# Performance work log

Measured on AMD Instinct MI355X. Metric: run time of the kernel, lower is better.

## Reference

```python
import jax, jax.numpy as jnp
import numpy as np

H = 1024   # hidden size
NH = 16    # num attention heads
HD = H // NH  # head dim = 64


def setup_inputs() -> dict:
    key = jax.random.key(0)
    ks = jax.random.split(key, 8)
    B, S = 2, 2048
    scale = 0.02
    return {
        "hidden_states": jax.random.normal(ks[0], (B, S, H), dtype=jnp.float32),
        "attention_mask": jnp.zeros((B, 1, 1, S), dtype=jnp.float32),
        "Wq": jax.random.normal(ks[1], (H, H), dtype=jnp.float32) * scale,
        "bq": jnp.zeros((H,), dtype=jnp.float32),
        "Wk": jax.random.normal(ks[2], (H, H), dtype=jnp.float32) * scale,
        "bk": jnp.zeros((H,), dtype=jnp.float32),
        "Wv": jax.random.normal(ks[3], (H, H), dtype=jnp.float32) * scale,
        "bv": jnp.zeros((H,), dtype=jnp.float32),
    }


def reference(hidden_states, attention_mask, Wq, bq, Wk, bk, Wv, bv):
    B, S, _ = hidden_states.shape

    def split_heads(x):  # [B,S,H] -> [B,NH,S,HD]
        return x.reshape(B, S, NH, HD).transpose(0, 2, 1, 3)

    q = split_heads(hidden_states @ Wq.T + bq)
    k = split_heads(hidden_states @ Wk.T + bk)
    v = split_heads(hidden_states @ Wv.T + bv)

    # raw attention scores [B,NH,S,S]
    scores = jnp.einsum("bhqd,bhkd->bhqk", q, k) / jnp.sqrt(jnp.float32(HD))
    scores = scores + attention_mask  # additive mask, broadcast [B,1,1,S]
    probs = jax.nn.softmax(scores, axis=-1)
    # dropout(p=0.1) is identity in eval mode

    ctx = jnp.einsum("bhqk,bhkd->bhqd", probs, v)  # [B,NH,S,HD]
    return ctx.transpose(0, 2, 1, 3).reshape(B, S, H)
```

## Files before the change

### kernel.cpp

```cpp
#include <hip/hip_runtime.h>
#include <hip/hip_bf16.h>
#include <math.h>

#define HSZ 1024
#define NHD 16
#define SEQ 2048
#define BSZ 2
#define MTOT (BSZ*SEQ)

typedef __attribute__((ext_vector_type(4)))  float  f32x4;
typedef __attribute__((ext_vector_type(8)))  __bf16 bf16x8;

#define LOG2E 1.4426950408889634f

#if __has_builtin(__builtin_amdgcn_exp2f)
#define EXP2(x) __builtin_amdgcn_exp2f(x)
#else
#define EXP2(x) exp2f(x)
#endif

__device__ __forceinline__ unsigned short f2bf(float x) {
    union { float f; unsigned u; } v; v.f = x;
    unsigned r = v.u + 0x7FFFu + ((v.u >> 16) & 1u);
    return (unsigned short)(r >> 16);
}
__device__ __forceinline__ unsigned cvtpk(float lo, float hi) {
    unsigned r;
    asm("v_cvt_pk_bf16_f32 %0, %1, %2" : "=v"(r) : "v"(lo), "v"(hi));
    return r;
}

__global__ __launch_bounds__(256) void cvt_all(
    const float* __restrict__ h,  unsigned short* __restrict__ hd,
    const float* __restrict__ w0, unsigned short* __restrict__ w0d,
    const float* __restrict__ w1, unsigned short* __restrict__ w1d,
    const float* __restrict__ w2, unsigned short* __restrict__ w2d)
{
    const float* s; unsigned short* d; int i;
    const int bid = blockIdx.x;
    if (bid < 2048)      { s = h;  d = hd;  i = bid; }
    else if (bid < 2560) { s = w0; d = w0d; i = bid - 2048; }
    else if (bid < 3072) { s = w1; d = w1d; i = bid - 2560; }
    else                 { s = w2; d = w2d; i = bid - 3072; }
    const int o = (i * 256 + threadIdx.x) * 8;
    float4 a = *(const float4*)(s + o);
    float4 b = *(const float4*)(s + o + 4);
    uint4 v;
    v.x = f2bf(a.x) | ((unsigned)f2bf(a.y) << 16);
    v.y = f2bf(a.z) | ((unsigned)f2bf(a.w) << 16);
    v.z = f2bf(b.x) | ((unsigned)f2bf(b.y) << 16);
    v.w = f2bf(b.z) | ((unsigned)f2bf(b.w) << 16);
    *(uint4*)(d + o) = v;
}

__global__ __launch_bounds__(256) void qkv_gemm(
    const unsigned short* __restrict__ hb,
    const unsigned short* __restrict__ wq,
    const unsigned short* __restrict__ wk,
    const unsigned short* __restrict__ wv,
    const float* __restrict__ bq, const float* __restrict__ bk,
    const float* __restrict__ bv,
    unsigned short* __restrict__ qo, char* __restrict__ ko,
    char* __restrict__ vo)
{
    __shared__ __align__(16) unsigned short As[128 * 32];
    __shared__ __align__(16) unsigned short Bs[128 * 32];

    const int t = threadIdx.x;
    const int w = t >> 6, l = t & 63, g = l >> 4, c = l & 15;
    const int bn = blockIdx.x, bm = blockIdx.y;
    const int which = bn >> 3;
    const int n0 = (bn & 7) << 7;
    const int m0 = bm << 7;
    const unsigned short* W = (which == 0) ? wq : (which == 1) ? wk : wv;
    const float* bb = (which == 0) ? bq : (which == 1) ? bk : bv;
    const float scale = (which == 0) ? 0.125f * LOG2E : 1.0f;
    const int wr = w >> 1, wc = w & 1;

    f32x4 acc[4][4];
    #pragma unroll
    for (int mi = 0; mi < 4; ++mi)
        #pragma unroll
        for (int ni = 0; ni < 4; ++ni) acc[mi][ni] = {0.f, 0.f, 0.f, 0.f};

    for (int k0 = 0; k0 < HSZ; k0 += 32) {
        #pragma unroll
        for (int i2 = 0; i2 < 2; ++i2) {
            const int chunk = 2 * w + i2;
            const int row = (chunk << 4) + (l >> 2);
            const int sg = (l & 3) ^ ((row >> 1) & 3);
            const char* ga = (const char*)hb +
                (((size_t)(m0 + row) << 10) + k0) * 2 + sg * 16;
            const char* gb = (const char*)W +
                (((size_t)(n0 + row) << 10) + k0) * 2 + sg * 16;
            __builtin_amdgcn_global_load_lds(
                (const __attribute__((address_space(1))) unsigned*)ga,
                (__attribute__((address_space(3))) unsigned*)((char*)As + chunk * 1024),
                16, 0, 0);
            __builtin_amdgcn_global_load_lds(
                (const __attribute__((address_space(1))) unsigned*)gb,
                (__attribute__((address_space(3))) unsigned*)((char*)Bs + chunk * 1024),
                16, 0, 0);
        }
        __syncthreads();

        bf16x8 af[4], bfr[4];
        #pragma unroll
        for (int mi = 0; mi < 4; ++mi) {
            const int row = wr * 64 + mi * 16 + c;
            const int gg = g ^ ((row >> 1) & 3);
            af[mi] = *(const bf16x8*)((const char*)As + row * 64 + gg * 16);
        }
        #pragma unroll
        for (int ni = 0; ni < 4; ++ni) {
            const int row = wc * 64 + ni * 16 + c;
            const int gg = g ^ ((row >> 1) & 3);
            bfr[ni] = *(const bf16x8*)((const char*)Bs + row * 64 + gg * 16);
        }
        #pragma unroll
        for (int mi = 0; mi < 4; ++mi)
            #pragma unroll
            for (int ni = 0; ni < 4; ++ni)
                acc[mi][ni] = __builtin_amdgcn_mfma_f32_16x16x32_bf16(
                    af[mi], bfr[ni], acc[mi][ni], 0, 0, 0);
        __syncthreads();
    }

    #pragma unroll
    for (int ni = 0; ni < 4; ++ni) {
        const int ncol = n0 + wc * 64 + ni * 16 + c;
        const int hh = ncol >> 6, d = ncol & 63;
        const float bsc = bb[ncol] * scale;
        #pragma unroll
        for (int mi = 0; mi < 4; ++mi) {
            #pragma unroll
            for (int j = 0; j < 4; ++j) {
                const int mrow = m0 + wr * 64 + mi * 16 + g * 4 + j;
                const int bi = mrow >> 11, si = mrow & 2047;
                const unsigned short val = f2bf(acc[mi][ni][j] * scale + bsc);
                const size_t bhoff = (size_t)(bi * NHD + hh);
                if (which == 0) {
                    qo[((bhoff * SEQ + si) << 6) + d] = val;
                } else if (which == 1) {
                    char* p = ko + (bhoff << 18) + ((size_t)(si >> 6) << 13)
                            + ((si & 63) << 7) + (((d << 1)) ^ ((si & 7) << 4));
                    *(unsigned short*)p = val;
                } else {
                    char* p = vo + (bhoff << 18) + ((size_t)(si >> 6) << 13)
                            + (d << 7) + (((si & 63) << 1) ^ ((d & 7) << 4));
                    *(unsigned short*)p = val;
                }
            }
        }
    }
}

__global__ __launch_bounds__(256) void attn_mfma(
    const unsigned short* __restrict__ qb, const char* __restrict__ kb,
    const char* __restrict__ vb, const float* __restrict__ mask,
    float* __restrict__ out)
{
    __shared__ __align__(16) char Kt[2][8192];
    __shared__ __align__(16) char Vt[2][8192];
    __shared__ __align__(16) unsigned Pl[4][16][32];

    const int t = threadIdx.x;
    const int w = t >> 6, l = t & 63, g = l >> 4, c = l & 15;
    const int qt = blockIdx.x, h = blockIdx.y, b = blockIdx.z;
    const int bh = b * NHD + h;
    const int q0 = qt * 64 + w * 16;

    const unsigned short* qp = qb + ((size_t)bh * SEQ + q0) * 64;
    const char* kbase = kb + ((size_t)bh << 18);
    const char* vbase = vb + ((size_t)bh << 18);
    const float* mp = mask + b * SEQ;

    bf16x8 qf[2];
    #pragma unroll
    for (int p = 0; p < 2; ++p)
        qf[p] = *(const bf16x8*)(qp + c * 64 + p * 32 + g * 8);

    f32x4 o[4];
    #pragma unroll
    for (int tt = 0; tt < 4; ++tt) o[tt] = {0.f, 0.f, 0.f, 0.f};
    f32x4 lacc = {0.f, 0.f, 0.f, 0.f};

    auto STAGE = [&](int tile, int buf) {
        const char* kg = kbase + tile * 8192 + w * 2048 + l * 16;
        const char* vg = vbase + tile * 8192 + w * 2048 + l * 16;
        #pragma unroll
        for (int i = 0; i < 2; ++i) {
            __builtin_amdgcn_global_load_lds(
                (const __attribute__((address_space(1))) unsigned*)(kg + i * 1024),
                (__attribute__((address_space(3))) unsigned*)(&Kt[buf][w * 2048 + i * 1024]),
                16, 0, 0);
            __builtin_amdgcn_global_load_lds(
                (const __attribute__((address_space(1))) unsigned*)(vg + i * 1024),
                (__attribute__((address_space(3))) unsigned*)(&Vt[buf][w * 2048 + i * 1024]),
                16, 0, 0);
        }
    };

    STAGE(0, 0);
    __syncthreads();

    for (int kt = 0; kt < 32; ++kt) {
        const int cur = kt & 1;
        const int kv0 = kt * 64;
        if (kt < 31) STAGE(kt + 1, cur ^ 1);

        bf16x8 kfr[4][2];
        #pragma unroll
        for (int t2 = 0; t2 < 4; ++t2)
            #pragma unroll
            for (int p = 0; p < 2; ++p)
                kfr[t2][p] = *(const bf16x8*)(&Kt[cur][(t2 * 16 + c) * 128
                                 + ((p * 64 + g * 16) ^ ((c & 7) << 4))]);

        f32x4 s[4];
        #pragma unroll
        for (int t2 = 0; t2 < 4; ++t2) s[t2] = {0.f, 0.f, 0.f, 0.f};
        __builtin_amdgcn_s_setprio(1);
        #pragma unroll
        for (int t2 = 0; t2 < 4; ++t2) {
            s[t2] = __builtin_amdgcn_mfma_f32_16x16x32_bf16(kfr[t2][0], qf[0], s[t2], 0, 0, 0);
            s[t2] = __builtin_amdgcn_mfma_f32_16x16x32_bf16(kfr[t2][1], qf[1], s[t2], 0, 0, 0);
        }
        __builtin_amdgcn_s_setprio(0);

        #pragma unroll
        for (int t2 = 0; t2 < 4; ++t2) {
            const float4 mv = *(const float4*)(mp + kv0 + t2 * 16 + g * 4);
            s[t2][0] = EXP2(fmaf(mv.x, LOG2E, s[t2][0]));
            s[t2][1] = EXP2(fmaf(mv.y, LOG2E, s[t2][1]));
            s[t2][2] = EXP2(fmaf(mv.z, LOG2E, s[t2][2]));
            s[t2][3] = EXP2(fmaf(mv.w, LOG2E, s[t2][3]));
            lacc[0] += s[t2][0]; lacc[1] += s[t2][1];
            lacc[2] += s[t2][2]; lacc[3] += s[t2][3];
        }

        #pragma unroll
        for (int t2 = 0; t2 < 4; ++t2) {
            uint2 pr;
            pr.x = cvtpk(s[t2][0], s[t2][1]);
            pr.y = cvtpk(s[t2][2], s[t2][3]);
            *(uint2*)&Pl[w][c][(8 * t2 + 2 * g) ^ ((c & 7) << 2)] = pr;
        }

        bf16x8 pfr[2];
        #pragma unroll
        for (int blk = 0; blk < 2; ++blk)
            pfr[blk] = *(const bf16x8*)&Pl[w][c][(16 * blk + 4 * g) ^ ((c & 7) << 2)];
        __builtin_amdgcn_s_setprio(1);
        #pragma unroll
        for (int tt = 0; tt < 4; ++tt) {
            #pragma unroll
            for (int blk = 0; blk < 2; ++blk) {
                const bf16x8 vfr = *(const bf16x8*)(&Vt[cur][(tt * 16 + c) * 128
                                     + ((blk * 64 + g * 16) ^ ((c & 7) << 4))]);
                o[tt] = __builtin_amdgcn_mfma_f32_16x16x32_bf16(vfr, pfr[blk], o[tt], 0, 0, 0);
            }
        }
        __builtin_amdgcn_s_setprio(0);

        __syncthreads();
    }

    float rs = (lacc[0] + lacc[1]) + (lacc[2] + lacc[3]);
    rs += __shfl_xor(rs, 16);
    rs += __shfl_xor(rs, 32);
    const float linv = 1.f / rs;

    #pragma unroll
    for (int tt = 0; tt < 4; ++tt) {
        const size_t rowb = ((size_t)(b * SEQ + q0 + c) << 10) + h * 64 + 16 * tt + 4 * g;
        out[rowb + 0] = o[tt][0] * linv;
        out[rowb + 1] = o[tt][1] * linv;
        out[rowb + 2] = o[tt][2] * linv;
        out[rowb + 3] = o[tt][3] * linv;
    }
}

extern "C" void kernel_launch(void* const* d_in, const int* in_sizes, int n_in,
                              void* d_out, int out_size, void* d_ws, size_t ws_size,
                              hipStream_t stream) {
    const float* hid  = (const float*)d_in[0];
    const float* mask = (const float*)d_in[1];
    const float* Wq   = (const float*)d_in[2];
    const float* bq   = (const float*)d_in[3];
    const float* Wk   = (const float*)d_in[4];
    const float* bk   = (const float*)d_in[5];
    const float* Wv   = (const float*)d_in[6];
    const float* bv   = (const float*)d_in[7];
    float* out = (float*)d_out;

    char* ws = (char*)d_ws;
    unsigned short* qbf = (unsigned short*)(ws);
    char*           kbf = ws + 8388608;
    char*           vbf = ws + 16777216;
    unsigned short* hbf = (unsigned short*)(ws + 25165824);
    unsigned short* wqb = (unsigned short*)(ws + 33554432);
    unsigned short* wkb = (unsigned short*)(ws + 35651584);
    unsigned short* wvb = (unsigned short*)(ws + 37748736);

    cvt_all<<<3584, 256, 0, stream>>>(hid, hbf, Wq, wqb, Wk, wkb, Wv, wvb);
    qkv_gemm<<<dim3(24, 32), 256, 0, stream>>>(hbf, wqb, wkb, wvb,
                                               bq, bk, bv, qbf, kbf, vbf);
    attn_mfma<<<dim3(32, NHD, BSZ), 256, 0, stream>>>(qbf, kbf, vbf, mask, out);
}
```

Before: 124.2 us.

## Fold mask into V, compute row sums via MFMA, deepen GEMM K-tile

Factors the additive mask out of the softmax exponent as a multiplicative exp(mask) term. It is applied to V in the QKV epilogue, and a bf16 exp(mask) vector is precomputed in the conversion kernel. The softmax denominator is then computed with an extra MFMA of exp(mask) against P, which removes the per-element mask loads, FMAs, row-sum adds and cross-lane shuffles from the attention inner loop. The QKV GEMM also doubles its K tile to 64 with a new 8-way LDS swizzle, halving the barrier count. Risks include bf16 rounding of exp(mask) in the denominator, and overflow or underflow when mask values are large negative, since exp(mask) may reach zero.

```diff
diff --git a/kernel.cpp b/kernel.cpp
--- a/kernel.cpp
+++ b/kernel.cpp
@@ -34,10 +34,23 @@
     const float* __restrict__ h,  unsigned short* __restrict__ hd,
     const float* __restrict__ w0, unsigned short* __restrict__ w0d,
     const float* __restrict__ w1, unsigned short* __restrict__ w1d,
-    const float* __restrict__ w2, unsigned short* __restrict__ w2d)
+    const float* __restrict__ w2, unsigned short* __restrict__ w2d,
+    const float* __restrict__ mask, unsigned short* __restrict__ mexpb)
 {
+    const int bid = blockIdx.x;
+    if (bid >= 3584) {
+        const int o = ((bid - 3584) * 256 + threadIdx.x) * 8;
+        float4 a = *(const float4*)(mask + o);
+        float4 b = *(const float4*)(mask + o + 4);
+        uint4 v;
+        v.x = f2bf(EXP2(a.x * LOG2E)) | ((unsigned)f2bf(EXP2(a.y * LOG2E)) << 16);
+        v.y = f2bf(EXP2(a.z * LOG2E)) | ((unsigned)f2bf(EXP2(a.w * LOG2E)) << 16);
+        v.z = f2bf(EXP2(b.x * LOG2E)) | ((unsigned)f2bf(EXP2(b.y * LOG2E)) << 16);
+        v.w = f2bf(EXP2(b.z * LOG2E)) | ((unsigned)f2bf(EXP2(b.w * LOG2E)) << 16);
+        *(uint4*)(mexpb + o) = v;
+        return;
+    }
     const float* s; unsigned short* d; int i;
-    const int bid = blockIdx.x;
     if (bid < 2048)      { s = h;  d = hd;  i = bid; }
     else if (bid < 2560) { s = w0; d = w0d; i = bid - 2048; }
     else if (bid < 3072) { s = w1; d = w1d; i = bid - 2560; }
@@ -59,12 +72,12 @@
     const unsigned short* __restrict__ wk,
     const unsigned short* __restrict__ wv,
     const float* __restrict__ bq, const float* __restrict__ bk,
-    const float* __restrict__ bv,
+    const float* __restrict__ bv, const float* __restrict__ mask,
     unsigned short* __restrict__ qo, char* __restrict__ ko,
     char* __restrict__ vo)
 {
-    __shared__ __align__(16) unsigned short As[128 * 32];
-    __shared__ __align__(16) unsigned short Bs[128 * 32];
+    __shared__ __align__(16) unsigned short As[128 * 64];
+    __shared__ __align__(16) unsigned short Bs[128 * 64];
 
     const int t = threadIdx.x;
     const int w = t >> 6, l = t & 63, g = l >> 4, c = l & 15;
@@ -83,46 +96,51 @@
         #pragma unroll
         for (int ni = 0; ni < 4; ++ni) acc[mi][ni] = {0.f, 0.f, 0.f, 0.f};
 
-    for (int k0 = 0; k0 < HSZ; k0 += 32) {
-        #pragma unroll
-        for (int i2 = 0; i2 < 2; ++i2) {
-            const int chunk = 2 * w + i2;
-            const int row = (chunk << 4) + (l >> 2);
-            const int sg = (l & 3) ^ ((row >> 1) & 3);
+    const int srow = l >> 3;
+    const int sg   = (l & 7) ^ (srow & 7);
+
+    for (int k0 = 0; k0 < HSZ; k0 += 64) {
+        #pragma unroll
+        for (int i3 = 0; i3 < 4; ++i3) {
+            const int chunk = 4 * w + i3;
+            const int row = chunk * 8 + srow;
             const char* ga = (const char*)hb +
                 (((size_t)(m0 + row) << 10) + k0) * 2 + sg * 16;
             const char* gb = (const char*)W +
                 (((size_t)(n0 + row) << 10) + k0) * 2 + sg * 16;
             __builtin_amdgcn_global_load_lds(
                 (const __attribute__((address_space(1))) unsigned*)ga,
-                (__attribute__((address_space(3))) unsigned*)((char*)As + chunk * 1024),
+                (__attribute__((address_space(3))) unsigned*)((char*)As + chunk * 1024 + (l & 63) * 16),
                 16, 0, 0);
             __builtin_amdgcn_global_load_lds(
                 (const __attribute__((address_space(1))) unsigned*)gb,
-                (__attribute__((address_space(3))) unsigned*)((char*)Bs + chunk * 1024),
+                (__attribute__((address_space(3))) unsigned*)((char*)Bs + chunk * 1024 + (l & 63) * 16),
                 16, 0, 0);
         }
         __syncthreads();
 
-        bf16x8 af[4], bfr[4];
-        #pragma unroll
-        for (int mi = 0; mi < 4; ++mi) {
-            const int row = wr * 64 + mi * 16 + c;
-            const int gg = g ^ ((row >> 1) & 3);
-            af[mi] = *(const bf16x8*)((const char*)As + row * 64 + gg * 16);
-        }
-        #pragma unroll
-        for (int ni = 0; ni < 4; ++ni) {
-            const int row = wc * 64 + ni * 16 + c;
-            const int gg = g ^ ((row >> 1) & 3);
-            bfr[ni] = *(const bf16x8*)((const char*)Bs + row * 64 + gg * 16);
-        }
-        #pragma unroll
-        for (int mi = 0; mi < 4; ++mi)
-            #pragma unroll
-            for (int ni = 0; ni < 4; ++ni)
-                acc[mi][ni] = __builtin_amdgcn_mfma_f32_16x16x32_bf16(
-                    af[mi], bfr[ni], acc[mi][ni], 0, 0, 0);
+        #pragma unroll
+        for (int kk = 0; kk < 2; ++kk) {
+            bf16x8 af[4], bfr[4];
+            #pragma unroll
+            for (int mi = 0; mi < 4; ++mi) {
+                const int row = wr * 64 + mi * 16 + c;
+                af[mi] = *(const bf16x8*)((const char*)As + row * 128
+                             + ((kk * 4 + g) ^ (row & 7)) * 16);
+            }
+            #pragma unroll
+            for (int ni = 0; ni < 4; ++ni) {
+                const int row = wc * 64 + ni * 16 + c;
+                bfr[ni] = *(const bf16x8*)((const char*)Bs + row * 128
+                             + ((kk * 4 + g) ^ (row & 7)) * 16);
+            }
+            #pragma unroll
+            for (int mi = 0; mi < 4; ++mi)
+                #pragma unroll
+                for (int ni = 0; ni < 4; ++ni)
+                    acc[mi][ni] = __builtin_amdgcn_mfma_f32_16x16x32_bf16(
+                        af[mi], bfr[ni], acc[mi][ni], 0, 0, 0);
+        }
         __syncthreads();
     }
 
@@ -137,18 +155,19 @@
             for (int j = 0; j < 4; ++j) {
                 const int mrow = m0 + wr * 64 + mi * 16 + g * 4 + j;
                 const int bi = mrow >> 11, si = mrow & 2047;
-                const unsigned short val = f2bf(acc[mi][ni][j] * scale + bsc);
+                float vf = acc[mi][ni][j] * scale + bsc;
                 const size_t bhoff = (size_t)(bi * NHD + hh);
                 if (which == 0) {
-                    qo[((bhoff * SEQ + si) << 6) + d] = val;
+                    qo[((bhoff * SEQ + si) << 6) + d] = f2bf(vf);
                 } else if (which == 1) {
                     char* p = ko + (bhoff << 18) + ((size_t)(si >> 6) << 13)
                             + ((si & 63) << 7) + (((d << 1)) ^ ((si & 7) << 4));
-                    *(unsigned short*)p = val;
+                    *(unsigned short*)p = f2bf(vf);
                 } else {
+                    vf *= EXP2(mask[bi * SEQ + si] * LOG2E);
                     char* p = vo + (bhoff << 18) + ((size_t)(si >> 6) << 13)
                             + (d << 7) + (((si & 63) << 1) ^ ((d & 7) << 4));
-                    *(unsigned short*)p = val;
+                    *(unsigned short*)p = f2bf(vf);
                 }
             }
         }
@@ -157,7 +176,7 @@
 
 __global__ __launch_bounds__(256) void attn_mfma(
     const unsigned short* __restrict__ qb, const char* __restrict__ kb,
-    const char* __restrict__ vb, const float* __restrict__ mask,
+    const char* __restrict__ vb, const unsigned short* __restrict__ mexpb,
     float* __restrict__ out)
 {
     __shared__ __align__(16) char Kt[2][8192];
@@ -173,7 +192,7 @@
     const unsigned short* qp = qb + ((size_t)bh * SEQ + q0) * 64;
     const char* kbase = kb + ((size_t)bh << 18);
     const char* vbase = vb + ((size_t)bh << 18);
-    const float* mp = mask + b * SEQ;
+    const unsigned short* mep = mexpb + b * SEQ;
 
     bf16x8 qf[2];
     #pragma unroll
@@ -183,7 +202,7 @@
     f32x4 o[4];
     #pragma unroll
     for (int tt = 0; tt < 4; ++tt) o[tt] = {0.f, 0.f, 0.f, 0.f};
-    f32x4 lacc = {0.f, 0.f, 0.f, 0.f};
+    f32x4 lsumacc = {0.f, 0.f, 0.f, 0.f};
 
     auto STAGE = [&](int tile, int buf) {
         const char* kg = kbase + tile * 8192 + w * 2048 + l * 16;
@@ -209,6 +228,11 @@
         const int kv0 = kt * 64;
         if (kt < 31) STAGE(kt + 1, cur ^ 1);
 
+        bf16x8 mf[2];
+        #pragma unroll
+        for (int blk = 0; blk < 2; ++blk)
+            mf[blk] = *(const bf16x8*)(mep + kv0 + blk * 32 + g * 8);
+
         bf16x8 kfr[4][2];
         #pragma unroll
         for (int t2 = 0; t2 < 4; ++t2)
@@ -230,13 +254,8 @@
 
         #pragma unroll
         for (int t2 = 0; t2 < 4; ++t2) {
-            const float4 mv = *(const float4*)(mp + kv0 + t2 * 16 + g * 4);
-            s[t2][0] = EXP2(fmaf(mv.x, LOG2E, s[t2][0]));
-            s[t2][1] = EXP2(fmaf(mv.y, LOG2E, s[t2][1]));
-            s[t2][2] = EXP2(fmaf(mv.z, LOG2E, s[t2][2]));
-            s[t2][3] = EXP2(fmaf(mv.w, LOG2E, s[t2][3]));
-            lacc[0] += s[t2][0]; lacc[1] += s[t2][1];
-            lacc[2] += s[t2][2]; lacc[3] += s[t2][3];
+            s[t2][0] = EXP2(s[t2][0]); s[t2][1] = EXP2(s[t2][1]);
+            s[t2][2] = EXP2(s[t2][2]); s[t2][3] = EXP2(s[t2][3]);
         }
 
         #pragma unroll
@@ -253,6 +272,9 @@
             pfr[blk] = *(const bf16x8*)&Pl[w][c][(16 * blk + 4 * g) ^ ((c & 7) << 2)];
         __builtin_amdgcn_s_setprio(1);
         #pragma unroll
+        for (int blk = 0; blk < 2; ++blk)
+            lsumacc = __builtin_amdgcn_mfma_f32_16x16x32_bf16(mf[blk], pfr[blk], lsumacc, 0, 0, 0);
+        #pragma unroll
         for (int tt = 0; tt < 4; ++tt) {
             #pragma unroll
             for (int blk = 0; blk < 2; ++blk) {
@@ -266,10 +288,7 @@
         __syncthreads();
     }
 
-    float rs = (lacc[0] + lacc[1]) + (lacc[2] + lacc[3]);
-    rs += __shfl_xor(rs, 16);
-    rs += __shfl_xor(rs, 32);
-    const float linv = 1.f / rs;
+    const float linv = 1.f / lsumacc[0];
 
     #pragma unroll
     for (int tt = 0; tt < 4; ++tt) {
@@ -302,9 +321,11 @@
     unsigned short* wqb = (unsigned short*)(ws + 33554432);
     unsigned short* wkb = (unsigned short*)(ws + 35651584);
     unsigned short* wvb = (unsigned short*)(ws + 37748736);
-
-    cvt_all<<<3584, 256, 0, stream>>>(hid, hbf, Wq, wqb, Wk, wkb, Wv, wvb);
+    unsigned short* mxb = (unsigned short*)(ws + 39845888);
+
+    cvt_all<<<3586, 256, 0, stream>>>(hid, hbf, Wq, wqb, Wk, wkb, Wv, wvb,
+                                      mask, mxb);
     qkv_gemm<<<dim3(24, 32), 256, 0, stream>>>(hbf, wqb, wkb, wvb,
-                                               bq, bk, bv, qbf, kbf, vbf);
-    attn_mfma<<<dim3(32, NHD, BSZ), 256, 0, stream>>>(qbf, kbf, vbf, mask, out);
-}
+                                               bq, bk, bv, mask, qbf, kbf, vbf);
+    attn_mfma<<<dim3(32, NHD, BSZ), 256, 0, stream>>>(qbf, kbf, vbf, mxb, out);
+}
```

Result: slower. 126.9 us (+2.1%).
